# Kernel optimization log

Hardware: AMD Instinct MI355X
Metric: run time of the kernel (lower is better)

Reference implementation:

```python
import jax, jax.numpy as jnp
import numpy as np

B, S, DIM, H, DH = 1, 8192, 2048, 32, 64
W = 128    # sliding window size
CBS = 64   # compress block size
NMEM = 4   # compressed memory kv
SCALE = DH ** -0.5


def setup_inputs() -> dict:
    key = jax.random.key(0)
    ks = jax.random.split(key, 12)
    di = H * DH
    f = lambda k, shape: jax.random.normal(k, shape, jnp.float32) * 0.02
    return dict(
        inp=jax.random.normal(ks[0], (B, S, DIM), jnp.float32),
        rms_w=jnp.ones((DIM,), jnp.float32),
        w_qkv=f(ks[1], (DIM, 3 * di)),
        k_pos=f(ks[2], (H, CBS, DH)),
        v_pos=f(ks[3], (H, CBS, DH)),
        kc_w=f(ks[4], (H, DH, DH, CBS)),   # grouped Conv1d weight per head: [h, d_out, d_in, kernel]
        kc_b=f(ks[5], (H, DH)),
        vc_w=f(ks[6], (H, DH, DH, CBS)),
        vc_b=f(ks[7], (H, DH)),
        mem_kv=f(ks[8], (2, H, NMEM, DH)),
        w_comb=f(ks[9], (DIM, 3 * H)),
        b_comb=jnp.zeros((3 * H,), jnp.float32),
        w_out=f(ks[10], (di, DIM)),
    )


def rms_norm(x, w):
    eps = jnp.finfo(x.dtype).eps
    return x * jax.lax.rsqrt(jnp.mean(x * x, axis=-1, keepdims=True) + eps) * w


def local_attention(q, k, v):
    # lucidrains LocalAttention: causal, look_backward=1, exact_windowsize -> allowed 0 <= i-j <= W
    b, h, n, d = q.shape
    nb = n // W
    qb = q.reshape(b, h, nb, W, d)
    kb = k.reshape(b, h, nb, W, d)
    vb = v.reshape(b, h, nb, W, d)
    prev = lambda t: jnp.concatenate([jnp.zeros_like(t[:, :, :1]), t[:, :, :-1]], axis=2)
    kk = jnp.concatenate([prev(kb), kb], axis=3)  # [b,h,nb,2W,d]
    vv = jnp.concatenate([prev(vb), vb], axis=3)
    sim = jnp.einsum('bhnid,bhnjd->bhnij', qb, kk) * SCALE
    qi = jnp.arange(nb)[:, None] * W + jnp.arange(W)[None, :]              # [nb,W] global query pos
    kj = (jnp.arange(nb)[:, None] - 1) * W + jnp.arange(2 * W)[None, :]    # [nb,2W] global key pos
    dist = qi[:, :, None] - kj[:, None, :]
    allowed = (dist >= 0) & (dist <= W) & (kj[:, None, :] >= 0)
    sim = jnp.where(allowed[None, None], sim, -jnp.finfo(sim.dtype).max)
    attn = jax.nn.softmax(sim, axis=-1)
    out = jnp.einsum('bhnij,bhnjd->bhnid', attn, vv)
    return out.reshape(b, h, n, d)


def reference(inp, rms_w, w_qkv, k_pos, v_pos, kc_w, kc_b, vc_w, vc_b, mem_kv, w_comb, b_comb, w_out):
    b, n, _ = inp.shape
    x = rms_norm(inp, rms_w)
    q, k, v = jnp.split(x @ w_qkv, 3, axis=-1)
    split = lambda t: t.reshape(b, n, H, DH).transpose(0, 2, 1, 3)  # b h n d
    q, k, v = split(q), split(k), split(v)

    # --- compressed branch (grouped strided conv == per-head block linear) ---
    nc = n // CBS
    kb = (k + jnp.tile(k_pos, (1, nc, 1))).reshape(b, H, nc, CBS, DH)
    vb = (v + jnp.tile(v_pos, (1, nc, 1))).reshape(b, H, nc, CBS, DH)
    ck = jnp.einsum('bhnti,hoit->bhno', kb, kc_w) + kc_b[None, :, None, :]
    cv = jnp.einsum('bhnti,hoit->bhno', vb, vc_w) + vc_b[None, :, None, :]
    ck = jnp.concatenate([jnp.broadcast_to(mem_kv[0], (b, H, NMEM, DH)), ck], axis=2)
    cv = jnp.concatenate([jnp.broadcast_to(mem_kv[1], (b, H, NMEM, DH)), cv], axis=2)
    csim = jnp.einsum('bhid,bhjd->bhij', q, ck) * SCALE
    cq_seq = jnp.arange(n)
    ck_seq = (jnp.arange(nc) + 1) * CBS - 1
    ck_seq = jnp.concatenate([jnp.full((NMEM,), -1, ck_seq.dtype), ck_seq])
    cmask = ck_seq[None, :] < cq_seq[:, None]  # faithful to source: mask where ck_seq[j] < cq_seq[i]
    csim = jnp.where(cmask[None, None], -jnp.finfo(csim.dtype).max, csim)
    cattn = jax.nn.softmax(csim, axis=-1)
    comp = jnp.einsum('bhij,bhjd->bhid', cattn, cv)

    # --- local sliding-window branch ---
    local = local_attention(q, k, v)

    # --- learned per-branch combine (source combines [local, local, compressed]) ---
    cw = jax.nn.sigmoid(x @ w_comb + b_comb).reshape(b, n, H, 3).transpose(0, 2, 1, 3)  # b h n 3
    out = (cw[..., 0:1] + cw[..., 1:2]) * local + cw[..., 2:3] * comp
    out = out.transpose(0, 2, 1, 3).reshape(b, n, H * DH)
    return out @ w_out
```

## Files before the change

### kernel.cpp

```cpp
#include <hip/hip_runtime.h>

typedef __bf16 bf16;
typedef __bf16 bf16x8 __attribute__((ext_vector_type(8)));
typedef float f32x4 __attribute__((ext_vector_type(4)));

typedef const __attribute__((address_space(1))) void* gas1p;
typedef __attribute__((address_space(3))) void* las3p;

#define DEV static __device__ __forceinline__

DEV void gload16(const void* g, void* l) {
  __builtin_amdgcn_global_load_lds((gas1p)g, (las3p)l, 16, 0, 0);
}

DEV f32x4 mfma16(bf16x8 a, bf16x8 b, f32x4 c) {
  return __builtin_amdgcn_mfma_f32_16x16x32_bf16(a, b, c, 0, 0, 0);
}

DEV f32x4 fzero4() { f32x4 z = {0.f, 0.f, 0.f, 0.f}; return z; }
DEV bf16x8 bzero8() {
  bf16x8 v;
#pragma unroll
  for (int e = 0; e < 8; ++e) v[e] = (bf16)0.f;
  return v;
}
DEV float sigm(float x) { return 1.f / (1.f + __expf(-x)); }

__global__ __launch_bounds__(256) void k_rmsnorm(const float* __restrict__ inp,
                                                 const float* __restrict__ w,
                                                 bf16* __restrict__ xb) {
  int n = blockIdx.x, tid = threadIdx.x;
  const float* row = inp + (size_t)n * 2048;
  float4 v0 = *(const float4*)(row + tid * 8);
  float4 v1 = *(const float4*)(row + tid * 8 + 4);
  float ss = v0.x * v0.x + v0.y * v0.y + v0.z * v0.z + v0.w * v0.w +
             v1.x * v1.x + v1.y * v1.y + v1.z * v1.z + v1.w * v1.w;
#pragma unroll
  for (int m = 1; m < 64; m <<= 1) ss += __shfl_xor(ss, m, 64);
  __shared__ float wsum[4];
  if ((tid & 63) == 0) wsum[tid >> 6] = ss;
  __syncthreads();
  float tot = wsum[0] + wsum[1] + wsum[2] + wsum[3];
  float scale = rsqrtf(tot * (1.0f / 2048.0f) + 1.1920928955078125e-07f);
  const float* wp = w + tid * 8;
  bf16* op = xb + (size_t)n * 2048 + tid * 8;
  float vals[8] = {v0.x, v0.y, v0.z, v0.w, v1.x, v1.y, v1.z, v1.w};
#pragma unroll
  for (int e = 0; e < 8; ++e) op[e] = (bf16)(vals[e] * scale * wp[e]);
}

__global__ __launch_bounds__(256) void k_transpose(const float* __restrict__ in,
                                                   bf16* __restrict__ out,
                                                   int R, int C, int Cout) {
  __shared__ float tile[32][33];
  int c0 = blockIdx.x * 32, r0 = blockIdx.y * 32;
  int tx = threadIdx.x & 31, ty = threadIdx.x >> 5;
#pragma unroll
  for (int i = 0; i < 4; ++i) {
    int r = r0 + ty + i * 8, c = c0 + tx;
    tile[ty + i * 8][tx] = (r < R && c < C) ? in[(size_t)r * C + c] : 0.0f;
  }
  __syncthreads();
#pragma unroll
  for (int i = 0; i < 4; ++i) {
    int c = c0 + ty + i * 8, r = r0 + tx;
    if (c < Cout && r < R) out[(size_t)c * R + r] = (bf16)tile[tx][ty + i * 8];
  }
}

__global__ __launch_bounds__(256) void k_convwT(const float* __restrict__ kcw,
                                                const float* __restrict__ vcw,
                                                bf16* __restrict__ bct) {
  int slab = blockIdx.x;
  const float* src = (slab < 2048 ? kcw : vcw) + (size_t)(slab & 2047) * 4096;
  bf16* dst = bct + (size_t)slab * 4096;
  __shared__ float t[64 * 65];
#pragma unroll
  for (int e = 0; e < 16; ++e) {
    int f = threadIdx.x + e * 256;
    t[(f >> 6) * 65 + (f & 63)] = src[f];
  }
  __syncthreads();
#pragma unroll
  for (int e = 0; e < 16; ++e) {
    int f = threadIdx.x + e * 256;
    dst[f] = (bf16)t[(f & 63) * 65 + (f >> 6)];
  }
}

template <typename OutT>
__global__ __launch_bounds__(256) void k_gemm(const bf16* __restrict__ A,
                                              const bf16* __restrict__ Bt,
                                              OutT* __restrict__ C,
                                              int M, int N, int K) {
  (void)M;
  __shared__ __align__(16) bf16 aT[128 * 32];
  __shared__ __align__(16) bf16 bT[128 * 32];
  int tid = threadIdx.x, wave = tid >> 6, lane = tid & 63;
  int bm = blockIdx.y, bn = blockIdx.x;
  int wm = (wave >> 1) * 64, wn = (wave & 1) * 64;
  int la = lane & 15, lk = (lane >> 4) * 8;
  f32x4 acc[4][4];
#pragma unroll
  for (int i = 0; i < 4; ++i)
#pragma unroll
    for (int j = 0; j < 4; ++j) acc[i][j] = fzero4();
  size_t aBase = (size_t)(bm * 128) * K, bBase = (size_t)(bn * 128) * K;
  const int nk = K >> 5;
  for (int kt = 0; kt < nk; ++kt) {
    int k0 = kt * 32;
    __syncthreads();
#pragma unroll
    for (int c = 0; c < 2; ++c) {
      int chunk = c * 256 + tid;
      int row = chunk >> 2, ko = (chunk & 3) * 8;
      gload16(A + aBase + (size_t)row * K + k0 + ko, aT + row * 32 + ko);
      gload16(Bt + bBase + (size_t)row * K + k0 + ko, bT + row * 32 + ko);
    }
    __syncthreads();
    bf16x8 af[4], bfr[4];
#pragma unroll
    for (int i = 0; i < 4; ++i) {
      af[i] = *(const bf16x8*)(aT + (wm + i * 16 + la) * 32 + lk);
      bfr[i] = *(const bf16x8*)(bT + (wn + i * 16 + la) * 32 + lk);
    }
#pragma unroll
    for (int i = 0; i < 4; ++i)
#pragma unroll
      for (int j = 0; j < 4; ++j) acc[i][j] = mfma16(af[i], bfr[j], acc[i][j]);
  }
  int rg = (lane >> 4) * 4;
#pragma unroll
  for (int i = 0; i < 4; ++i)
#pragma unroll
    for (int j = 0; j < 4; ++j)
#pragma unroll
      for (int v = 0; v < 4; ++v) {
        int r = bm * 128 + wm + i * 16 + rg + v;
        int col = bn * 128 + wn + j * 16 + la;
        C[(size_t)r * N + col] = (OutT)acc[i][j][v];
      }
}

__global__ __launch_bounds__(256) void k_convgemm(const bf16* __restrict__ qkv,
                                                  const float* __restrict__ kpos,
                                                  const float* __restrict__ vpos,
                                                  const float* __restrict__ kcb,
                                                  const float* __restrict__ vcb,
                                                  const bf16* __restrict__ bct,
                                                  bf16* __restrict__ ckbuf) {
  int kv = blockIdx.x >> 5, h = blockIdx.x & 31;
  const float* pos = kv ? vpos : kpos;
  const float* bias = kv ? vcb : kcb;
  int koff = 2048 + kv * 2048;
  __shared__ __align__(16) bf16 bT[64 * 32];
  int tid = threadIdx.x, wave = tid >> 6, lane = tid & 63;
  int la = lane & 15, lg = lane >> 4;
  f32x4 acc[2][4];
#pragma unroll
  for (int i = 0; i < 2; ++i)
#pragma unroll
    for (int j = 0; j < 4; ++j) acc[i][j] = fzero4();
  const bf16* bsrc = bct + (size_t)((kv * 32 + h) * 64) * 4096;
  for (int kt = 0; kt < 128; ++kt) {
    __syncthreads();
    gload16(bsrc + (size_t)(tid >> 2) * 4096 + kt * 32 + (tid & 3) * 8,
            bT + (tid >> 2) * 32 + (tid & 3) * 8);
    __syncthreads();
    int t = kt >> 1;
    int i0 = (kt & 1) * 32 + lg * 8;
    bf16x8 bf4[4];
#pragma unroll
    for (int j = 0; j < 4; ++j) bf4[j] = *(const bf16x8*)(bT + (j * 16 + la) * 32 + lg * 8);
#pragma unroll
    for (int mi = 0; mi < 2; ++mi) {
      int jrow = wave * 32 + mi * 16 + la;
      int n = jrow * 64 + t;
      bf16x8 qv = *(const bf16x8*)(qkv + (size_t)n * 6144 + koff + h * 64 + i0);
      const float* pp = pos + h * 4096 + t * 64 + i0;
      bf16x8 a;
#pragma unroll
      for (int e = 0; e < 8; ++e) a[e] = (bf16)((float)qv[e] + pp[e]);
#pragma unroll
      for (int j = 0; j < 4; ++j) acc[mi][j] = mfma16(a, bf4[j], acc[mi][j]);
    }
  }
  bf16* dst = ckbuf + (size_t)((kv * 32 + h) * 160) * 64;
#pragma unroll
  for (int mi = 0; mi < 2; ++mi)
#pragma unroll
    for (int j = 0; j < 4; ++j)
#pragma unroll
      for (int v = 0; v < 4; ++v) {
        int jr = wave * 32 + mi * 16 + lg * 4 + v;
        int o = j * 16 + la;
        dst[(size_t)(4 + jr) * 64 + o] = (bf16)(acc[mi][j][v] + bias[h * 64 + o]);
      }
}

__global__ __launch_bounds__(256) void k_fillck(const float* __restrict__ memkv,
                                                bf16* __restrict__ ckbuf) {
  int kv = blockIdx.x >> 5, h = blockIdx.x & 31;
  bf16* dst = ckbuf + (size_t)((kv * 32 + h) * 160) * 64;
  int tid = threadIdx.x;
  dst[tid] = (bf16)memkv[(size_t)(kv * 32 + h) * 256 + tid];
  for (int f = tid; f < 28 * 64; f += 256) dst[132 * 64 + f] = (bf16)0.f;
}

__global__ __launch_bounds__(512) void k_local(const bf16* __restrict__ qkv,
                                               bf16* __restrict__ lout) {
  int qb = blockIdx.x, h = blockIdx.y;
  __shared__ __align__(16) bf16 kl[256 * 72];
  __shared__ __align__(16) bf16 vT[64 * 264];
  __shared__ __align__(16) bf16 pl[128 * 264];
  int tid = threadIdx.x, wave = tid >> 6, lane = tid & 63;
  int la = lane & 15, lg = lane >> 4;
#pragma unroll
  for (int it = 0; it < 4; ++it) {
    int c = it * 512 + tid;
    int row = c >> 3, off = (c & 7) * 8;
    int n = qb * 128 - 128 + row;
    bf16x8 kvr = bzero8(), vvr = bzero8();
    if (n >= 0) {
      kvr = *(const bf16x8*)(qkv + (size_t)n * 6144 + 2048 + h * 64 + off);
      vvr = *(const bf16x8*)(qkv + (size_t)n * 6144 + 4096 + h * 64 + off);
    }
    *(bf16x8*)(kl + row * 72 + off) = kvr;
#pragma unroll
    for (int e = 0; e < 8; ++e) vT[(off + e) * 264 + row] = vvr[e];
  }
  int nq = qb * 128 + wave * 16 + la;
  bf16x8 aq0 = *(const bf16x8*)(qkv + (size_t)nq * 6144 + h * 64 + lg * 8);
  bf16x8 aq1 = *(const bf16x8*)(qkv + (size_t)nq * 6144 + h * 64 + 32 + lg * 8);
  __syncthreads();
  f32x4 s[16];
#pragma unroll
  for (int nf = 0; nf < 16; ++nf) {
    bf16x8 b0 = *(const bf16x8*)(kl + (nf * 16 + la) * 72 + lg * 8);
    bf16x8 b1 = *(const bf16x8*)(kl + (nf * 16 + la) * 72 + 32 + lg * 8);
    f32x4 t = fzero4();
    t = mfma16(aq0, b0, t);
    t = mfma16(aq1, b1, t);
    s[nf] = t;
  }
  float mx[4] = {-1e30f, -1e30f, -1e30f, -1e30f};
#pragma unroll
  for (int nf = 0; nf < 16; ++nf)
#pragma unroll
    for (int v = 0; v < 4; ++v) {
      int iq = wave * 16 + lg * 4 + v;
      int jj = nf * 16 + la;
      bool ok = (jj >= iq) && (jj <= iq + 128) && (qb > 0 || jj >= 128);
      float sv = ok ? s[nf][v] * 0.125f : -1e30f;
      s[nf][v] = sv;
      mx[v] = fmaxf(mx[v], sv);
    }
#pragma unroll
  for (int v = 0; v < 4; ++v)
#pragma unroll
    for (int m = 1; m < 16; m <<= 1) mx[v] = fmaxf(mx[v], __shfl_xor(mx[v], m, 64));
  float den[4] = {0.f, 0.f, 0.f, 0.f};
#pragma unroll
  for (int nf = 0; nf < 16; ++nf)
#pragma unroll
    for (int v = 0; v < 4; ++v) {
      float p = __expf(s[nf][v] - mx[v]);
      s[nf][v] = p;
      den[v] += p;
    }
#pragma unroll
  for (int v = 0; v < 4; ++v)
#pragma unroll
    for (int m = 1; m < 16; m <<= 1) den[v] += __shfl_xor(den[v], m, 64);
#pragma unroll
  for (int nf = 0; nf < 16; ++nf)
#pragma unroll
    for (int v = 0; v < 4; ++v)
      pl[(wave * 16 + lg * 4 + v) * 264 + nf * 16 + la] = (bf16)s[nf][v];
  __syncthreads();
  bf16x8 ap[8];
#pragma unroll
  for (int kk = 0; kk < 8; ++kk)
    ap[kk] = *(const bf16x8*)(pl + (wave * 16 + la) * 264 + kk * 32 + lg * 8);
  f32x4 o[4];
#pragma unroll
  for (int j = 0; j < 4; ++j) o[j] = fzero4();
#pragma unroll
  for (int j = 0; j < 4; ++j)
#pragma unroll
    for (int kk = 0; kk < 8; ++kk) {
      bf16x8 b = *(const bf16x8*)(vT + (j * 16 + la) * 264 + kk * 32 + lg * 8);
      o[j] = mfma16(ap[kk], b, o[j]);
    }
#pragma unroll
  for (int j = 0; j < 4; ++j)
#pragma unroll
    for (int v = 0; v < 4; ++v) {
      int n = qb * 128 + wave * 16 + lg * 4 + v;
      int d = j * 16 + la;
      lout[(size_t)n * 2048 + h * 64 + d] = (bf16)(o[j][v] / den[v]);
    }
}

__global__ __launch_bounds__(512) void k_comp(const bf16* __restrict__ qkv,
                                              const bf16* __restrict__ ckbuf,
                                              bf16* __restrict__ cout) {
  int qb = blockIdx.x, h = blockIdx.y;
  __shared__ __align__(16) bf16 ckl[160 * 72];
  __shared__ __align__(16) bf16 cvT[64 * 168];
  __shared__ __align__(16) bf16 pl[128 * 168];
  int tid = threadIdx.x, wave = tid >> 6, lane = tid & 63;
  int la = lane & 15, lg = lane >> 4;
  const bf16* cks = ckbuf + (size_t)(h * 160) * 64;
  const bf16* cvs = ckbuf + (size_t)((32 + h) * 160) * 64;
  for (int c = tid; c < 1280; c += 512) {
    int row = c >> 3, off = (c & 7) * 8;
    *(bf16x8*)(ckl + row * 72 + off) = *(const bf16x8*)(cks + row * 64 + off);
    bf16x8 vv = *(const bf16x8*)(cvs + row * 64 + off);
#pragma unroll
    for (int e = 0; e < 8; ++e) cvT[(off + e) * 168 + row] = vv[e];
  }
  int nq = qb * 128 + wave * 16 + la;
  bf16x8 aq0 = *(const bf16x8*)(qkv + (size_t)nq * 6144 + h * 64 + lg * 8);
  bf16x8 aq1 = *(const bf16x8*)(qkv + (size_t)nq * 6144 + h * 64 + 32 + lg * 8);
  __syncthreads();
  f32x4 s[10];
#pragma unroll
  for (int nf = 0; nf < 10; ++nf) {
    bf16x8 b0 = *(const bf16x8*)(ckl + (nf * 16 + la) * 72 + lg * 8);
    bf16x8 b1 = *(const bf16x8*)(ckl + (nf * 16 + la) * 72 + 32 + lg * 8);
    f32x4 t = fzero4();
    t = mfma16(aq0, b0, t);
    t = mfma16(aq1, b1, t);
    s[nf] = t;
  }
  int bi = qb * 2 + (wave >> 2);
  float mx[4] = {-1e30f, -1e30f, -1e30f, -1e30f};
#pragma unroll
  for (int nf = 0; nf < 10; ++nf)
#pragma unroll
    for (int v = 0; v < 4; ++v) {
      int jj = nf * 16 + la;
      bool ok = (jj >= 4 + bi) && (jj < 132);
      float sv = ok ? s[nf][v] * 0.125f : -1e30f;
      s[nf][v] = sv;
      mx[v] = fmaxf(mx[v], sv);
    }
#pragma unroll
  for (int v = 0; v < 4; ++v)
#pragma unroll
    for (int m = 1; m < 16; m <<= 1) mx[v] = fmaxf(mx[v], __shfl_xor(mx[v], m, 64));
  float den[4] = {0.f, 0.f, 0.f, 0.f};
#pragma unroll
  for (int nf = 0; nf < 10; ++nf)
#pragma unroll
    for (int v = 0; v < 4; ++v) {
      float p = __expf(s[nf][v] - mx[v]);
      s[nf][v] = p;
      den[v] += p;
    }
#pragma unroll
  for (int v = 0; v < 4; ++v)
#pragma unroll
    for (int m = 1; m < 16; m <<= 1) den[v] += __shfl_xor(den[v], m, 64);
#pragma unroll
  for (int nf = 0; nf < 10; ++nf)
#pragma unroll
    for (int v = 0; v < 4; ++v)
      pl[(wave * 16 + lg * 4 + v) * 168 + nf * 16 + la] = (bf16)s[nf][v];
  __syncthreads();
  bf16x8 ap[5];
#pragma unroll
  for (int kk = 0; kk < 5; ++kk)
    ap[kk] = *(const bf16x8*)(pl + (wave * 16 + la) * 168 + kk * 32 + lg * 8);
  f32x4 o[4];
#pragma unroll
  for (int j = 0; j < 4; ++j) o[j] = fzero4();
#pragma unroll
  for (int j = 0; j < 4; ++j)
#pragma unroll
    for (int kk = 0; kk < 5; ++kk) {
      bf16x8 b = *(const bf16x8*)(cvT + (j * 16 + la) * 168 + kk * 32 + lg * 8);
      o[j] = mfma16(ap[kk], b, o[j]);
    }
#pragma unroll
  for (int j = 0; j < 4; ++j)
#pragma unroll
    for (int v = 0; v < 4; ++v) {
      int n = qb * 128 + wave * 16 + lg * 4 + v;
      int d = j * 16 + la;
      cout[(size_t)n * 2048 + h * 64 + d] = (bf16)(o[j][v] / den[v]);
    }
}

__global__ __launch_bounds__(256) void k_combine(const bf16* __restrict__ lo,
                                                 const bf16* __restrict__ co,
                                                 const float* __restrict__ comb,
                                                 const float* __restrict__ bcomb,
                                                 bf16* __restrict__ att) {
  size_t idx = (size_t)blockIdx.x * 256 + threadIdx.x;
  size_t base = idx * 8;
  int n = (int)(base >> 11);
  int hd = (int)(base & 2047);
  int h = hd >> 6;
  const float* cb = comb + (size_t)n * 128 + h * 3;
  float s0 = sigm(cb[0] + bcomb[h * 3 + 0]);
  float s1 = sigm(cb[1] + bcomb[h * 3 + 1]);
  float s2 = sigm(cb[2] + bcomb[h * 3 + 2]);
  float wl = s0 + s1;
  bf16x8 l = *(const bf16x8*)(lo + base);
  bf16x8 c = *(const bf16x8*)(co + base);
  bf16x8 r;
#pragma unroll
  for (int e = 0; e < 8; ++e) r[e] = (bf16)(wl * (float)l[e] + s2 * (float)c[e]);
  *(bf16x8*)(att + base) = r;
}

extern "C" void kernel_launch(void* const* d_in, const int* in_sizes, int n_in,
                              void* d_out, int out_size, void* d_ws, size_t ws_size,
                              hipStream_t stream) {
  const float* inp = (const float*)d_in[0];
  const float* rmsw = (const float*)d_in[1];
  const float* wqkv = (const float*)d_in[2];
  const float* kpos = (const float*)d_in[3];
  const float* vpos = (const float*)d_in[4];
  const float* kcw = (const float*)d_in[5];
  const float* kcb = (const float*)d_in[6];
  const float* vcw = (const float*)d_in[7];
  const float* vcb = (const float*)d_in[8];
  const float* memkv = (const float*)d_in[9];
  const float* wcomb = (const float*)d_in[10];
  const float* bcomb = (const float*)d_in[11];
  const float* wout = (const float*)d_in[12];
  float* out = (float*)d_out;

  char* ws = (char*)d_ws;
  size_t off = 0;
  auto alloc = [&](size_t bytes) {
    void* p = ws + off;
    off += (bytes + 255) & ~(size_t)255;
    return p;
  };
  bf16* qkv = (bf16*)alloc(100663296);
  bf16* regX = (bf16*)alloc(33554432);
  bf16* regT1 = (bf16*)alloc(33554432);
  bf16* regT2 = (bf16*)alloc(33554432);
  bf16* woutT = (bf16*)alloc(8388608);
  bf16* wcombT = (bf16*)alloc(524288);
  bf16* ckbuf = (bf16*)alloc(1310720);
  float* combb = (float*)alloc(4194304);

  bf16* xb = regX;
  bf16* wqkvT = regT1;
  bf16* bct = regT2;

  k_rmsnorm<<<8192, 256, 0, stream>>>(inp, rmsw, xb);
  k_transpose<<<dim3(192, 64), 256, 0, stream>>>(wqkv, wqkvT, 2048, 6144, 6144);
  k_transpose<<<dim3(64, 64), 256, 0, stream>>>(wout, woutT, 2048, 2048, 2048);
  k_transpose<<<dim3(4, 64), 256, 0, stream>>>(wcomb, wcombT, 2048, 96, 128);
  k_convwT<<<4096, 256, 0, stream>>>(kcw, vcw, bct);
  k_gemm<bf16><<<dim3(48, 64), 256, 0, stream>>>(xb, wqkvT, qkv, 8192, 6144, 2048);
  k_gemm<float><<<dim3(1, 64), 256, 0, stream>>>(xb, wcombT, combb, 8192, 128, 2048);
  k_fillck<<<64, 256, 0, stream>>>(memkv, ckbuf);
  k_convgemm<<<64, 256, 0, stream>>>(qkv, kpos, vpos, kcb, vcb, bct, ckbuf);
  bf16* lout = regT2;
  k_local<<<dim3(64, 32), 512, 0, stream>>>(qkv, lout);
  bf16* cout = regT1;
  k_comp<<<dim3(64, 32), 512, 0, stream>>>(qkv, ckbuf, cout);
  bf16* att = regX;
  k_combine<<<8192, 256, 0, stream>>>(lout, cout, combb, bcomb, att);
  k_gemm<float><<<dim3(16, 64), 256, 0, stream>>>(att, woutT, out, 8192, 2048, 2048);
  (void)in_sizes; (void)n_in; (void)out_size; (void)ws_size;
}
```

Before: 907.2 us.

## Add 256x256 pipelined GEMM kernel for QKV and output projections

Introduces a new GEMM kernel with 256x256 output tiles, 512 threads, and K-step 64. It double-buffers the A and B tiles in LDS (128KB), loading them with direct global-to-LDS transfers. LDS is XOR-swizzled to avoid bank conflicts, the work-group order is swizzled for L2 locality, and it uses a four-phase MFMA schedule with raised wave priority. The aim is more data reuse per tile and overlap of loads with compute in the two large projections. The cost is heavier LDS and register use, which limits occupancy, and the 256 blocks for the output GEMM may underfill the GPU's CUs.

```diff
diff --git a/kernel.cpp b/kernel.cpp
--- a/kernel.cpp
+++ b/kernel.cpp
@@ -140,6 +140,138 @@
         int col = bn * 128 + wn + j * 16 + la;
         C[(size_t)r * N + col] = (OutT)acc[i][j][v];
       }
+}
+
+DEV bf16x8 ldsfrag(const char* slot, int row, int ks, int lg) {
+  int off = (row << 7) + ((((ks << 6) | (lg << 4))) ^ ((row & 7) << 4));
+  return *(const bf16x8*)(slot + off);
+}
+
+#define READ_A(SLOT)                                                      \
+  _Pragma("unroll") for (int m_ = 0; m_ < 4; ++m_)                        \
+      _Pragma("unroll") for (int ks_ = 0; ks_ < 2; ++ks_)                 \
+          afr[m_][ks_] = ldsfrag(SLOT, wr64 + m_ * 16 + la, ks_, lg);
+
+#define READ_B(SLOT)                                                      \
+  _Pragma("unroll") for (int n_ = 0; n_ < 2; ++n_)                        \
+      _Pragma("unroll") for (int ks_ = 0; ks_ < 2; ++ks_)                 \
+          bfr[n_][ks_] = ldsfrag(SLOT, wc32 + n_ * 16 + la, ks_, lg);
+
+#define MFMA_PHASE(MQ, NQ)                                                \
+  __builtin_amdgcn_s_setprio(1);                                          \
+  _Pragma("unroll") for (int m_ = 0; m_ < 4; ++m_)                        \
+      _Pragma("unroll") for (int n_ = 0; n_ < 2; ++n_)                    \
+          _Pragma("unroll") for (int ks_ = 0; ks_ < 2; ++ks_) acc[MQ][NQ] \
+              [m_][n_] = mfma16(afr[m_][ks_], bfr[n_][ks_],               \
+                                acc[MQ][NQ][m_][n_]);                     \
+  __builtin_amdgcn_s_setprio(0);
+
+#define BAR() __builtin_amdgcn_s_barrier()
+
+template <typename OutT>
+__global__ __launch_bounds__(512, 2) void k_gemm256(const bf16* __restrict__ A,
+                                                    const bf16* __restrict__ Bt,
+                                                    OutT* __restrict__ C,
+                                                    int M, int N, int K) {
+  (void)M;
+  __shared__ __align__(16) char LB[131072];
+  const int tid = threadIdx.x;
+  const int lane = tid & 63, wave = tid >> 6;
+  const int la = lane & 15, lg = lane >> 4;
+  const int wr64 = (wave >> 2) * 64, wc32 = (wave & 3) * 32;
+  const int nbn = N >> 8;
+  const int nwg = gridDim.x, wg = blockIdx.x;
+  const int swz = (wg & 7) * (nwg >> 3) + (wg >> 3);
+  const int bm = swz / nbn, bn = swz % nbn;
+  const int NK = K >> 6;
+
+  const bf16* aT0 = A + (size_t)(bm * 256) * K;
+  const bf16* aT1 = A + (size_t)(bm * 256 + 128) * K;
+  const bf16* bT0 = Bt + (size_t)(bn * 256) * K;
+  const bf16* bT1 = Bt + (size_t)(bn * 256 + 128) * K;
+  const int g1 = tid + 512;
+  const size_t sOff0 = (size_t)(tid >> 3) * K + (((tid & 7) ^ ((tid >> 3) & 7)) << 3);
+  const size_t sOff1 = (size_t)(g1 >> 3) * K + (((g1 & 7) ^ ((g1 >> 3) & 7)) << 3);
+  const int dOff0 = tid * 16, dOff1 = g1 * 16;
+  char* AS = LB;
+  char* BS = LB + 65536;
+
+  auto stage = [&](const bf16* base, int kt, char* slot) {
+    gload16(base + sOff0 + kt * 64, slot + dOff0);
+    gload16(base + sOff1 + kt * 64, slot + dOff1);
+  };
+
+  f32x4 acc[2][2][4][2];
+#pragma unroll
+  for (int a = 0; a < 2; ++a)
+#pragma unroll
+    for (int b = 0; b < 2; ++b)
+#pragma unroll
+      for (int m = 0; m < 4; ++m)
+#pragma unroll
+        for (int n = 0; n < 2; ++n) acc[a][b][m][n] = fzero4();
+
+  stage(aT0, 0, AS + 0 * 16384);
+  stage(aT1, 0, AS + 1 * 16384);
+  stage(bT0, 0, BS + 0 * 16384);
+  stage(bT1, 0, BS + 1 * 16384);
+  stage(aT0, 1, AS + 2 * 16384);
+  stage(bT0, 1, BS + 2 * 16384);
+  asm volatile("s_waitcnt vmcnt(4)" ::: "memory");
+  BAR();
+
+  bf16x8 afr[4][2], bfr[2][2];
+  for (int kt = 0; kt < NK; ++kt) {
+    const int par = kt & 1;
+    char* aCur0 = AS + (par * 2 + 0) * 16384;
+    char* aCur1 = AS + (par * 2 + 1) * 16384;
+    char* bCur0 = BS + (par * 2 + 0) * 16384;
+    char* bCur1 = BS + (par * 2 + 1) * 16384;
+    char* aNxt1 = AS + ((par ^ 1) * 2 + 1) * 16384;
+    char* bNxt1 = BS + ((par ^ 1) * 2 + 1) * 16384;
+    READ_A(aCur0);
+    READ_B(bCur0);
+    if (kt + 1 < NK) stage(aT1, kt + 1, aNxt1);
+    BAR();
+    MFMA_PHASE(0, 0);
+    BAR();
+    READ_B(bCur1);
+    if (kt + 1 < NK) stage(bT1, kt + 1, bNxt1);
+    BAR();
+    MFMA_PHASE(0, 1);
+    BAR();
+    READ_A(aCur1);
+    READ_B(bCur0);
+    if (kt + 2 < NK) stage(aT0, kt + 2, aCur0);
+    BAR();
+    MFMA_PHASE(1, 0);
+    BAR();
+    READ_B(bCur1);
+    if (kt + 2 < NK) stage(bT0, kt + 2, bCur0);
+    BAR();
+    MFMA_PHASE(1, 1);
+    if (kt < NK - 2) {
+      asm volatile("s_waitcnt vmcnt(4)" ::: "memory");
+    } else {
+      asm volatile("s_waitcnt vmcnt(0)" ::: "memory");
+    }
+    BAR();
+  }
+
+#pragma unroll
+  for (int mq = 0; mq < 2; ++mq)
+#pragma unroll
+    for (int nq = 0; nq < 2; ++nq)
+#pragma unroll
+      for (int m = 0; m < 4; ++m)
+#pragma unroll
+        for (int n = 0; n < 2; ++n)
+#pragma unroll
+          for (int v = 0; v < 4; ++v) {
+            int row = bm * 256 + mq * 128 + wr64 + m * 16 + lg * 4 + v;
+            int col = bn * 256 + nq * 128 + wc32 + n * 16 + la;
+            C[(size_t)row * N + col] = (OutT)acc[mq][nq][m][n][v];
+          }
 }
 
 __global__ __launch_bounds__(256) void k_convgemm(const bf16* __restrict__ qkv,
@@ -459,7 +591,7 @@
   k_transpose<<<dim3(64, 64), 256, 0, stream>>>(wout, woutT, 2048, 2048, 2048);
   k_transpose<<<dim3(4, 64), 256, 0, stream>>>(wcomb, wcombT, 2048, 96, 128);
   k_convwT<<<4096, 256, 0, stream>>>(kcw, vcw, bct);
-  k_gemm<bf16><<<dim3(48, 64), 256, 0, stream>>>(xb, wqkvT, qkv, 8192, 6144, 2048);
+  k_gemm256<bf16><<<768, 512, 0, stream>>>(xb, wqkvT, qkv, 8192, 6144, 2048);
   k_gemm<float><<<dim3(1, 64), 256, 0, stream>>>(xb, wcombT, combb, 8192, 128, 2048);
   k_fillck<<<64, 256, 0, stream>>>(memkv, ckbuf);
   k_convgemm<<<64, 256, 0, stream>>>(qkv, kpos, vpos, kcb, vcb, bct, ckbuf);
@@ -469,6 +601,6 @@
   k_comp<<<dim3(64, 32), 512, 0, stream>>>(qkv, ckbuf, cout);
   bf16* att = regX;
   k_combine<<<8192, 256, 0, stream>>>(lout, cout, combb, bcomb, att);
-  k_gemm<float><<<dim3(16, 64), 256, 0, stream>>>(att, woutT, out, 8192, 2048, 2048);
+  k_gemm256<float><<<256, 512, 0, stream>>>(att, woutT, out, 8192, 2048, 2048);
   (void)in_sizes; (void)n_in; (void)out_size; (void)ws_size;
 }
```

New measurement: 812.3 us. -10.5%, faster.
